# Optimization experiments

Measured on AMD Instinct MI355X. Metric: run time of the kernel, lower is better.

Reference implementation:

```python
import jax, jax.numpy as jnp
import numpy as np

B, L, D, H, E = 8, 256, 128, 6, 32

def setup_inputs() -> dict:
    key = jax.random.key(0)
    ks = jax.random.split(key, 9)
    s = 0.02
    return {
        "x": jax.random.normal(ks[0], (B, L, D), jnp.float32),
        "weight_adj": jax.random.uniform(ks[1], (B, H, L, L), jnp.float32),
        "e": jax.random.normal(ks[2], (B, L, L, E), jnp.float32),
        "W_w": jax.random.normal(ks[3], (D, D), jnp.float32) * s,
        "W_b": jax.random.normal(ks[4], (D,), jnp.float32) * s,
        "Wx_w": jax.random.normal(ks[5], (H, H + 2 * D + E), jnp.float32) * s,
        "Wx_b": jax.random.normal(ks[6], (H,), jnp.float32) * s,
        "Wxx_w": jax.random.normal(ks[7], (D, D), jnp.float32) * s,
        "Wxx_b": jax.random.normal(ks[8], (D,), jnp.float32) * s,
    }

def reference(x, weight_adj, e, W_w, W_b, Wx_w, Wx_b, Wxx_w, Wxx_b):
    d = x.shape[-1]
    h = weight_adj.shape[1]
    # mean over heads, then graph conv + linear + relu
    adj_avg = weight_adj.mean(axis=1)                      # [B,L,L]
    gcn = jax.nn.relu(jnp.einsum('bij,bjd->bid', adj_avg, x) @ W_w.T + W_b)  # [B,L,d]
    # Wx applied to cat([weight_adj_perm, node_i, node_j, e], -1), decomposed
    # column-wise so the huge [B,L,L,2d+H+E] concat is never materialized;
    # math is identical to Linear(cat(...)).
    Wa  = Wx_w[:, :h]                 # [H,H]
    Wn1 = Wx_w[:, h:h + d]            # [H,d]
    Wn2 = Wx_w[:, h + d:h + 2 * d]    # [H,d]
    We  = Wx_w[:, h + 2 * d:]         # [H,E]
    adj_term = jnp.einsum('bhij,kh->bijk', weight_adj, Wa)   # [B,L,L,H]
    n1 = gcn @ Wn1.T                                          # [B,L,H] (row node)
    n2 = gcn @ Wn2.T                                          # [B,L,H] (col node)
    e_term = jnp.einsum('bije,ke->bijk', e, We)               # [B,L,L,H]
    new_adj = adj_term + n1[:, :, None, :] + n2[:, None, :, :] + e_term + Wx_b
    new_adj = jnp.transpose(new_adj, (0, 3, 1, 2))            # [B,H,L,L]
    out = gcn @ Wxx_w.T + Wxx_b                               # [B,L,d]
    return out, new_adj
```

## Files before the change

### kernel.cpp

```cpp
#include <hip/hip_runtime.h>

#define Bn 8
#define Ln 256
#define Dn 128
#define Hn 6
#define En 32
#define WXROW (Hn + 2*Dn + En)
#define ROWS 8

__global__ __launch_bounds__(128) void k_gcn(
    const float* __restrict__ x, const float* __restrict__ wadj,
    const float* __restrict__ W_w, const float* __restrict__ W_b,
    const float* __restrict__ Wx_w,
    const float* __restrict__ Wxx_w, const float* __restrict__ Wxx_b,
    float* __restrict__ out, float* __restrict__ n1_ws, float* __restrict__ n2_ws)
{
    __shared__ float adj[ROWS][Ln];
    __shared__ float t_s[ROWS][Dn];
    __shared__ float g_s[ROWS][Dn];

    const int t  = threadIdx.x;
    const int b  = blockIdx.x >> 5;
    const int i0 = (blockIdx.x & 31) * ROWS;

    const float inv_h = 1.0f / 6.0f;
    for (int idx = t; idx < ROWS * Ln; idx += 128) {
        const int r = idx >> 8, jj = idx & 255;
        float s = 0.f;
        #pragma unroll
        for (int h = 0; h < Hn; ++h)
            s += wadj[(((size_t)b * Hn + h) * Ln + (i0 + r)) * Ln + jj];
        adj[r][jj] = s * inv_h;
    }
    __syncthreads();

    {
        float acc[ROWS];
        #pragma unroll
        for (int r = 0; r < ROWS; ++r) acc[r] = 0.f;
        const float* xp = x + (size_t)b * Ln * Dn + t;
        #pragma unroll 4
        for (int j = 0; j < Ln; ++j) {
            const float xv = xp[(size_t)j * Dn];
            #pragma unroll
            for (int r = 0; r < ROWS; ++r)
                acc[r] = fmaf(adj[r][j], xv, acc[r]);
        }
        #pragma unroll
        for (int r = 0; r < ROWS; ++r) t_s[r][t] = acc[r];
    }
    __syncthreads();

    {
        float acc[ROWS];
        const float bias = W_b[t];
        #pragma unroll
        for (int r = 0; r < ROWS; ++r) acc[r] = bias;
        const float4* wr = (const float4*)(W_w + (size_t)t * Dn);
        #pragma unroll 8
        for (int c = 0; c < Dn / 4; ++c) {
            const float4 w = wr[c];
            const int base = c * 4;
            #pragma unroll
            for (int r = 0; r < ROWS; ++r) {
                float a = acc[r];
                a = fmaf(t_s[r][base + 0], w.x, a);
                a = fmaf(t_s[r][base + 1], w.y, a);
                a = fmaf(t_s[r][base + 2], w.z, a);
                a = fmaf(t_s[r][base + 3], w.w, a);
                acc[r] = a;
            }
        }
        #pragma unroll
        for (int r = 0; r < ROWS; ++r) g_s[r][t] = fmaxf(acc[r], 0.f);
    }
    __syncthreads();

    {
        float acc[ROWS];
        const float bias = Wxx_b[t];
        #pragma unroll
        for (int r = 0; r < ROWS; ++r) acc[r] = bias;
        const float4* wr = (const float4*)(Wxx_w + (size_t)t * Dn);
        #pragma unroll 8
        for (int c = 0; c < Dn / 4; ++c) {
            const float4 w = wr[c];
            const int base = c * 4;
            #pragma unroll
            for (int r = 0; r < ROWS; ++r) {
                float a = acc[r];
                a = fmaf(g_s[r][base + 0], w.x, a);
                a = fmaf(g_s[r][base + 1], w.y, a);
                a = fmaf(g_s[r][base + 2], w.z, a);
                a = fmaf(g_s[r][base + 3], w.w, a);
                acc[r] = a;
            }
        }
        #pragma unroll
        for (int r = 0; r < ROWS; ++r)
            out[((size_t)b * Ln + (i0 + r)) * Dn + t] = acc[r];
    }

    if (t < ROWS * 2 * Hn) {
        const int r  = t / (2 * Hn);
        const int kk = t % (2 * Hn);
        const int k  = (kk < Hn) ? kk : (kk - Hn);
        const bool isn2 = (kk >= Hn);
        const float* wrow = Wx_w + (size_t)k * WXROW + Hn + (isn2 ? Dn : 0);
        float acc = 0.f;
        #pragma unroll 8
        for (int c = 0; c < Dn; ++c)
            acc = fmaf(g_s[r][c], wrow[c], acc);
        const size_t idx = ((size_t)b * Hn + k) * Ln + (i0 + r);
        if (isn2) n2_ws[idx] = acc;
        else      n1_ws[idx] = acc;
    }
}

__global__ __launch_bounds__(256) void k_adj(
    const float* __restrict__ wadj, const float* __restrict__ e,
    const float* __restrict__ Wx_w, const float* __restrict__ Wx_b,
    const float* __restrict__ n1_ws, const float* __restrict__ n2_ws,
    float* __restrict__ new_adj)
{
    __shared__ float Wa_s[Hn][Hn];
    __shared__ float We_s[Hn][En];
    __shared__ float bias_n1[Hn];

    const int t = threadIdx.x;
    const int b = blockIdx.x >> 8;
    const int i = blockIdx.x & 255;

    if (t < Hn * Hn) {
        const int k = t / Hn, h = t % Hn;
        Wa_s[k][h] = Wx_w[(size_t)k * WXROW + h];
    }
    if (t >= 64 && t < 64 + Hn * En) {
        const int q = t - 64, k = q / En, c = q % En;
        We_s[k][c] = Wx_w[(size_t)k * WXROW + Hn + 2 * Dn + c];
    }
    if (t >= 32 && t < 32 + Hn) {
        const int k = t - 32;
        bias_n1[k] = Wx_b[k] + n1_ws[((size_t)b * Hn + k) * Ln + i];
    }
    __syncthreads();

    const int j = t;

    float ev[En];
    {
        const float4* ep = (const float4*)(e + (((size_t)b * Ln + i) * Ln + j) * En);
        #pragma unroll
        for (int c = 0; c < En / 4; ++c) {
            const float4 v = ep[c];
            ev[c * 4 + 0] = v.x;
            ev[c * 4 + 1] = v.y;
            ev[c * 4 + 2] = v.z;
            ev[c * 4 + 3] = v.w;
        }
    }

    float wv[Hn];
    #pragma unroll
    for (int h = 0; h < Hn; ++h)
        wv[h] = wadj[(((size_t)b * Hn + h) * Ln + i) * Ln + j];

    float n2v[Hn];
    #pragma unroll
    for (int k = 0; k < Hn; ++k)
        n2v[k] = n2_ws[((size_t)b * Hn + k) * Ln + j];

    #pragma unroll
    for (int k = 0; k < Hn; ++k) {
        float acc = bias_n1[k] + n2v[k];
        #pragma unroll
        for (int h = 0; h < Hn; ++h)
            acc = fmaf(wv[h], Wa_s[k][h], acc);
        #pragma unroll
        for (int c = 0; c < En; ++c)
            acc = fmaf(ev[c], We_s[k][c], acc);
        new_adj[(((size_t)b * Hn + k) * Ln + i) * Ln + j] = acc;
    }
}

extern "C" void kernel_launch(void* const* d_in, const int* in_sizes, int n_in,
                              void* d_out, int out_size, void* d_ws, size_t ws_size,
                              hipStream_t stream) {
    const float* x      = (const float*)d_in[0];
    const float* wadj   = (const float*)d_in[1];
    const float* e      = (const float*)d_in[2];
    const float* W_w    = (const float*)d_in[3];
    const float* W_b    = (const float*)d_in[4];
    const float* Wx_w   = (const float*)d_in[5];
    const float* Wx_b   = (const float*)d_in[6];
    const float* Wxx_w  = (const float*)d_in[7];
    const float* Wxx_b  = (const float*)d_in[8];

    float* out      = (float*)d_out;
    float* new_adj  = out + (size_t)Bn * Ln * Dn;

    float* n1_ws = (float*)d_ws;
    float* n2_ws = n1_ws + (size_t)Bn * Hn * Ln;

    k_gcn<<<Bn * (Ln / ROWS), 128, 0, stream>>>(x, wadj, W_w, W_b, Wx_w,
                                                Wxx_w, Wxx_b, out, n1_ws, n2_ws);
    k_adj<<<Bn * Ln, 256, 0, stream>>>(wadj, e, Wx_w, Wx_b, n1_ws, n2_ws, new_adj);
}
```

Baseline: 174.9 us.

## Split GCN reduction across 256 threads and stage e tiles through padded LDS

k_gcn now processes 4 rows per block with 256 threads. The j-reduction is split into two halves whose partial sums are combined in shared memory, and each thread computes two output rows, which doubles the block count and parallelism for the small GCN stage. k_adj now loads each block's e slab with coalesced float4 reads into a padded LDS buffer, instead of each thread reading its own 128-byte strided run. The cost is about 33 KB of LDS per k_adj block, which may lower occupancy, plus an extra sync and combine step in k_gcn.

Measured after the change: 154.3 us. 1.13x faster.

```diff
diff --git a/kernel.cpp b/kernel.cpp
--- a/kernel.cpp
+++ b/kernel.cpp
@@ -6,9 +6,9 @@
 #define Hn 6
 #define En 32
 #define WXROW (Hn + 2*Dn + En)
-#define ROWS 8
-
-__global__ __launch_bounds__(128) void k_gcn(
+#define ROWS 4
+
+__global__ __launch_bounds__(256) void k_gcn(
     const float* __restrict__ x, const float* __restrict__ wadj,
     const float* __restrict__ W_w, const float* __restrict__ W_b,
     const float* __restrict__ Wx_w,
@@ -16,21 +16,26 @@
     float* __restrict__ out, float* __restrict__ n1_ws, float* __restrict__ n2_ws)
 {
     __shared__ float adj[ROWS][Ln];
+    __shared__ float part[2][ROWS][Dn];
     __shared__ float t_s[ROWS][Dn];
     __shared__ float g_s[ROWS][Dn];
 
     const int t  = threadIdx.x;
-    const int b  = blockIdx.x >> 5;
-    const int i0 = (blockIdx.x & 31) * ROWS;
+    const int s  = t >> 7;
+    const int d  = t & 127;
+    const int b  = blockIdx.x >> 6;
+    const int i0 = (blockIdx.x & 63) * ROWS;
 
     const float inv_h = 1.0f / 6.0f;
-    for (int idx = t; idx < ROWS * Ln; idx += 128) {
+    #pragma unroll
+    for (int rep = 0; rep < ROWS; ++rep) {
+        const int idx = t + rep * 256;
         const int r = idx >> 8, jj = idx & 255;
-        float s = 0.f;
+        float sum = 0.f;
         #pragma unroll
         for (int h = 0; h < Hn; ++h)
-            s += wadj[(((size_t)b * Hn + h) * Ln + (i0 + r)) * Ln + jj];
-        adj[r][jj] = s * inv_h;
+            sum += wadj[(((size_t)b * Hn + h) * Ln + (i0 + r)) * Ln + jj];
+        adj[r][jj] = sum * inv_h;
     }
     __syncthreads();
 
@@ -38,67 +43,69 @@
         float acc[ROWS];
         #pragma unroll
         for (int r = 0; r < ROWS; ++r) acc[r] = 0.f;
-        const float* xp = x + (size_t)b * Ln * Dn + t;
+        const float* xp = x + (size_t)b * Ln * Dn + d;
+        const int j0 = s * 128;
         #pragma unroll 4
-        for (int j = 0; j < Ln; ++j) {
+        for (int jj = 0; jj < 128; ++jj) {
+            const int j = j0 + jj;
             const float xv = xp[(size_t)j * Dn];
             #pragma unroll
             for (int r = 0; r < ROWS; ++r)
                 acc[r] = fmaf(adj[r][j], xv, acc[r]);
         }
         #pragma unroll
-        for (int r = 0; r < ROWS; ++r) t_s[r][t] = acc[r];
-    }
-    __syncthreads();
-
-    {
-        float acc[ROWS];
-        const float bias = W_b[t];
-        #pragma unroll
-        for (int r = 0; r < ROWS; ++r) acc[r] = bias;
-        const float4* wr = (const float4*)(W_w + (size_t)t * Dn);
+        for (int r = 0; r < ROWS; ++r) part[s][r][d] = acc[r];
+    }
+    __syncthreads();
+
+    {
+        const int r0 = s, r1 = s + 2;
+        t_s[r0][d] = part[0][r0][d] + part[1][r0][d];
+        t_s[r1][d] = part[0][r1][d] + part[1][r1][d];
+    }
+    __syncthreads();
+
+    {
+        const int r0 = s, r1 = s + 2;
+        float a0 = W_b[d], a1 = a0;
+        const float4* wr = (const float4*)(W_w + (size_t)d * Dn);
         #pragma unroll 8
-        for (int c = 0; c < Dn / 4; ++c) {
-            const float4 w = wr[c];
-            const int base = c * 4;
-            #pragma unroll
-            for (int r = 0; r < ROWS; ++r) {
-                float a = acc[r];
-                a = fmaf(t_s[r][base + 0], w.x, a);
-                a = fmaf(t_s[r][base + 1], w.y, a);
-                a = fmaf(t_s[r][base + 2], w.z, a);
-                a = fmaf(t_s[r][base + 3], w.w, a);
-                acc[r] = a;
-            }
-        }
-        #pragma unroll
-        for (int r = 0; r < ROWS; ++r) g_s[r][t] = fmaxf(acc[r], 0.f);
-    }
-    __syncthreads();
-
-    {
-        float acc[ROWS];
-        const float bias = Wxx_b[t];
-        #pragma unroll
-        for (int r = 0; r < ROWS; ++r) acc[r] = bias;
-        const float4* wr = (const float4*)(Wxx_w + (size_t)t * Dn);
+        for (int c4 = 0; c4 < Dn / 4; ++c4) {
+            const float4 w = wr[c4];
+            const int c = c4 * 4;
+            a0 = fmaf(t_s[r0][c+0], w.x, a0);
+            a0 = fmaf(t_s[r0][c+1], w.y, a0);
+            a0 = fmaf(t_s[r0][c+2], w.z, a0);
+            a0 = fmaf(t_s[r0][c+3], w.w, a0);
+            a1 = fmaf(t_s[r1][c+0], w.x, a1);
+            a1 = fmaf(t_s[r1][c+1], w.y, a1);
+            a1 = fmaf(t_s[r1][c+2], w.z, a1);
+            a1 = fmaf(t_s[r1][c+3], w.w, a1);
+        }
+        g_s[r0][d] = fmaxf(a0, 0.f);
+        g_s[r1][d] = fmaxf(a1, 0.f);
+    }
+    __syncthreads();
+
+    {
+        const int r0 = s, r1 = s + 2;
+        float a0 = Wxx_b[d], a1 = a0;
+        const float4* wr = (const float4*)(Wxx_w + (size_t)d * Dn);
         #pragma unroll 8
-        for (int c = 0; c < Dn / 4; ++c) {
-            const float4 w = wr[c];
-            const int base = c * 4;
-            #pragma unroll
-            for (int r = 0; r < ROWS; ++r) {
-                float a = acc[r];
-                a = fmaf(g_s[r][base + 0], w.x, a);
-                a = fmaf(g_s[r][base + 1], w.y, a);
-                a = fmaf(g_s[r][base + 2], w.z, a);
-                a = fmaf(g_s[r][base + 3], w.w, a);
-                acc[r] = a;
-            }
-        }
-        #pragma unroll
-        for (int r = 0; r < ROWS; ++r)
-            out[((size_t)b * Ln + (i0 + r)) * Dn + t] = acc[r];
+        for (int c4 = 0; c4 < Dn / 4; ++c4) {
+            const float4 w = wr[c4];
+            const int c = c4 * 4;
+            a0 = fmaf(g_s[r0][c+0], w.x, a0);
+            a0 = fmaf(g_s[r0][c+1], w.y, a0);
+            a0 = fmaf(g_s[r0][c+2], w.z, a0);
+            a0 = fmaf(g_s[r0][c+3], w.w, a0);
+            a1 = fmaf(g_s[r1][c+0], w.x, a1);
+            a1 = fmaf(g_s[r1][c+1], w.y, a1);
+            a1 = fmaf(g_s[r1][c+2], w.z, a1);
+            a1 = fmaf(g_s[r1][c+3], w.w, a1);
+        }
+        out[((size_t)b * Ln + (i0 + r0)) * Dn + d] = a0;
+        out[((size_t)b * Ln + (i0 + r1)) * Dn + d] = a1;
     }
 
     if (t < ROWS * 2 * Hn) {
@@ -117,12 +124,14 @@
     }
 }
 
+#define EPAD 33
 __global__ __launch_bounds__(256) void k_adj(
     const float* __restrict__ wadj, const float* __restrict__ e,
     const float* __restrict__ Wx_w, const float* __restrict__ Wx_b,
     const float* __restrict__ n1_ws, const float* __restrict__ n2_ws,
     float* __restrict__ new_adj)
 {
+    __shared__ float e_lds[Ln * EPAD];
     __shared__ float Wa_s[Hn][Hn];
     __shared__ float We_s[Hn][En];
     __shared__ float bias_n1[Hn];
@@ -143,21 +152,28 @@
         const int k = t - 32;
         bias_n1[k] = Wx_b[k] + n1_ws[((size_t)b * Hn + k) * Ln + i];
     }
+
+    {
+        const float4* ep4 = (const float4*)(e + (((size_t)b * Ln + i) * Ln) * En);
+        #pragma unroll
+        for (int k = 0; k < 8; ++k) {
+            const int idx = t + k * 256;
+            const float4 v = ep4[idx];
+            const int j = idx >> 3;
+            const int c = (idx & 7) * 4;
+            float* dst = &e_lds[j * EPAD + c];
+            dst[0] = v.x; dst[1] = v.y; dst[2] = v.z; dst[3] = v.w;
+        }
+    }
     __syncthreads();
 
     const int j = t;
 
     float ev[En];
     {
-        const float4* ep = (const float4*)(e + (((size_t)b * Ln + i) * Ln + j) * En);
-        #pragma unroll
-        for (int c = 0; c < En / 4; ++c) {
-            const float4 v = ep[c];
-            ev[c * 4 + 0] = v.x;
-            ev[c * 4 + 1] = v.y;
-            ev[c * 4 + 2] = v.z;
-            ev[c * 4 + 3] = v.w;
-        }
+        const float* src = &e_lds[j * EPAD];
+        #pragma unroll
+        for (int c = 0; c < En; ++c) ev[c] = src[c];
     }
 
     float wv[Hn];
@@ -202,7 +218,7 @@
     float* n1_ws = (float*)d_ws;
     float* n2_ws = n1_ws + (size_t)Bn * Hn * Ln;
 
-    k_gcn<<<Bn * (Ln / ROWS), 128, 0, stream>>>(x, wadj, W_w, W_b, Wx_w,
+    k_gcn<<<Bn * (Ln / ROWS), 256, 0, stream>>>(x, wadj, W_w, W_b, Wx_w,
                                                 Wxx_w, Wxx_b, out, n1_ws, n2_ws);
     k_adj<<<Bn * Ln, 256, 0, stream>>>(wadj, e, Wx_w, Wx_b, n1_ws, n2_ws, new_adj);
 }
```
